# Performance work log

Hardware: AMD Instinct MI355X
Metric: run time of the kernel (lower is better)

The kernel has to match this reference:

```python
import jax, jax.numpy as jnp
import numpy as np

B, T, H = 4096, 2048, 64  # batch, max seq len, hidden size
IN = 1                    # decoder input hardcoded to width 1 in source
BOT = 3                   # latent bottleneck (linear_enc: H->3, linear_dec: 3->H)


def setup_inputs() -> dict:
    key = jax.random.key(0)
    ks = jax.random.split(key, 16)
    s = 1.0 / np.sqrt(H)
    u = lambda k, shape: jax.random.uniform(k, shape, jnp.float32, -s, s)
    padded = jax.random.normal(ks[0], (B, T, IN), jnp.float32)
    seq_lengths = jax.random.randint(ks[1], (B,), 1, T + 1).at[0].set(T)  # max == T (static unroll)
    return {
        "padded": padded,
        "seq_lengths": seq_lengths,
        # encoder LSTM (gate order i,f,g,o like torch); biases b_ih+b_hh fused
        "enc_Wih": u(ks[2], (4 * H, IN)),
        "enc_Whh": u(ks[3], (4 * H, H)),
        "enc_b":   u(ks[4], (4 * H,)),
        # encoder bottleneck linear H->3
        "enc_linW": u(ks[5], (BOT, H)),
        "enc_linb": u(ks[6], (BOT,)),
        # decoder expand linear 3->H
        "dec_linW": u(ks[7], (H, BOT)),
        "dec_linb": u(ks[8], (H,)),
        # decoder LSTM
        "dec_Wih": u(ks[9], (4 * H, IN)),
        "dec_Whh": u(ks[10], (4 * H, H)),
        "dec_b":   u(ks[11], (4 * H,)),
        # output linear H->1
        "outW": u(ks[12], (IN, H)),
        "outb": u(ks[13], (IN,)),
    }


def _lstm_cell(x, h, c, Wih, Whh, b):
    g = x @ Wih.T + h @ Whh.T + b
    i, f, gg, o = jnp.split(g, 4, axis=-1)
    c = jax.nn.sigmoid(f) * c + jax.nn.sigmoid(i) * jnp.tanh(gg)
    h = jax.nn.sigmoid(o) * jnp.tanh(c)
    return h, c


def reference(padded, seq_lengths, enc_Wih, enc_Whh, enc_b, enc_linW, enc_linb,
              dec_linW, dec_linb, dec_Wih, dec_Whh, dec_b, outW, outb):
    Bn, Tn, _ = padded.shape
    Hn = enc_Whh.shape[1]
    xs = jnp.transpose(padded, (1, 0, 2))                       # (T, B, 1)
    mask = jnp.arange(Tn)[:, None] < seq_lengths[None, :]        # (T, B)

    # ---- encoder: packed semantics == freeze (h,c) past each seq's length ----
    h0 = jnp.zeros((Bn, Hn), padded.dtype)
    def enc_step(carry, xm):
        h, c = carry
        x, m = xm
        nh, nc = _lstm_cell(x, h, c, enc_Wih, enc_Whh, enc_b)
        m = m[:, None]
        return (jnp.where(m, nh, h), jnp.where(m, nc, c)), None
    (h, c), _ = jax.lax.scan(enc_step, (h0, h0), (xs, mask))

    hz = jax.nn.sigmoid(h @ enc_linW.T + enc_linb)               # (B, 3) latent

    hd = hz @ dec_linW.T + dec_linb                              # (B, H)
    x0 = jnp.zeros((Bn, 1), padded.dtype)
    def dec_step(carry, _):
        x, hh, cc = carry
        nh, nc = _lstm_cell(x, hh, cc, dec_Wih, dec_Whh, dec_b)
        y = nh @ outW.T + outb
        return (y, nh, nc), y
    _, ys = jax.lax.scan(dec_step, (x0, hd, c), None, length=Tn)  # (T, B, 1)
    output = jnp.transpose(ys, (1, 0, 2))                         # (B, T, 1)

    # ---- masked MSE ----
    maskf = mask.T[:, :, None].astype(padded.dtype)               # (B, T, 1)
    loss = (((padded - output) ** 2) * maskf).sum() / maskf.sum()
    return loss, padded, output, hz[None]
```

## Files before the change

### kernel.cpp

```cpp
#include <hip/hip_runtime.h>

#define B 4096
#define T 2048
#define H 64
#define NBATCH 16
#define NB (B / NBATCH)
#define NTHREADS 512

typedef __attribute__((ext_vector_type(8))) short short8;
typedef __attribute__((ext_vector_type(4))) float f32x4;

__device__ __forceinline__ float ex2(float x) { return __builtin_amdgcn_exp2f(x); }
__device__ __forceinline__ float sigm(float x) {
    return __builtin_amdgcn_rcpf(1.0f + ex2(-1.4426950408889634f * x));
}
__device__ __forceinline__ float tanh_(float x) {
    return __builtin_fmaf(2.0f,
        __builtin_amdgcn_rcpf(1.0f + ex2(-2.8853900817779268f * x)), -1.0f);
}
__device__ __forceinline__ unsigned short f2bf(float f) {
    unsigned u = __builtin_bit_cast(unsigned, f);
    u += 0x7fffu + ((u >> 16) & 1u);
    return (unsigned short)(u >> 16);
}
__device__ __forceinline__ unsigned pk_bf16(float a, float b) {
    unsigned r;
    asm("v_cvt_pk_bf16_f32 %0, %1, %2" : "=v"(r) : "v"(a), "v"(b));
    return r;
}
__device__ __forceinline__ void lds_barrier() {
    asm volatile("s_waitcnt lgkmcnt(0)\n\ts_barrier" ::: "memory");
}

extern "C" __global__ void __launch_bounds__(NTHREADS, 2)
enc_kernel(const float* __restrict__ padded, const int* __restrict__ seq_len,
           const float* __restrict__ Wih, const float* __restrict__ Whh,
           const float* __restrict__ bias,
           float* __restrict__ h_out, float* __restrict__ c_out)
{
    __shared__ unsigned short hX[2][NBATCH][72];
    __shared__ int slen[NBATCH];

    const int tid = threadIdx.x;
    const int w = tid >> 6, L = tid & 63, lo = L & 15, hi = L >> 4;
    const int b0 = blockIdx.x * NBATCH;
    const int unitA = w * 8 + hi;
    const int unitB = w * 8 + 4 + hi;

    short8 af[2][2];
    #pragma unroll
    for (int rt = 0; rt < 2; ++rt) {
        const int G = (lo & 3) * 64 + w * 8 + rt * 4 + (lo >> 2);
        #pragma unroll
        for (int kk = 0; kk < 2; ++kk) {
            const float* src = Whh + (long)G * H + kk * 32 + hi * 8;
            short8 f;
            #pragma unroll
            for (int j = 0; j < 8; ++j) f[j] = (short)f2bf(src[j]);
            af[rt][kk] = f;
        }
    }
    float b_g[2][4], wi_g[2][4];
    #pragma unroll
    for (int rt = 0; rt < 2; ++rt)
        #pragma unroll
        for (int r = 0; r < 4; ++r) {
            const int G2 = r * 64 + w * 8 + rt * 4 + hi;
            b_g[rt][r] = bias[G2];
            wi_g[rt][r] = Wih[G2];
        }

    #pragma unroll
    for (int idx = tid; idx < NBATCH * 64; idx += NTHREADS)
        hX[0][idx >> 6][idx & 63] = 0;
    if (tid < NBATCH) slen[tid] = seq_len[b0 + tid];
    lds_barrier();

    int maxlen = 1;
    #pragma unroll
    for (int i = 0; i < NBATCH; ++i) maxlen = max(maxlen, slen[i]);
    const int len_lo = slen[lo];

    const float* xrow = padded + (long)(b0 + lo) * T;
    f32x4 xc = *(const f32x4*)(xrow);
    f32x4 xn = *(const f32x4*)(xrow + 4);

    float csA = 0.f, hsA = 0.f, csB = 0.f, hsB = 0.f;

#define ESTEP(P, XI)                                                          \
    {                                                                         \
        const float x = xc[XI];                                               \
        short8 hb0 = *(const short8*)&hX[P][lo][hi * 8];                      \
        short8 hb1 = *(const short8*)&hX[P][lo][32 + hi * 8];                 \
        f32x4 z0 = {b_g[0][0] + wi_g[0][0] * x, b_g[0][1] + wi_g[0][1] * x,   \
                    b_g[0][2] + wi_g[0][2] * x, b_g[0][3] + wi_g[0][3] * x};  \
        f32x4 z1 = {b_g[1][0] + wi_g[1][0] * x, b_g[1][1] + wi_g[1][1] * x,   \
                    b_g[1][2] + wi_g[1][2] * x, b_g[1][3] + wi_g[1][3] * x};  \
        z0 = __builtin_amdgcn_mfma_f32_16x16x32_bf16(af[0][0], hb0, z0, 0,0,0); \
        z1 = __builtin_amdgcn_mfma_f32_16x16x32_bf16(af[1][0], hb0, z1, 0,0,0); \
        z0 = __builtin_amdgcn_mfma_f32_16x16x32_bf16(af[0][1], hb1, z0, 0,0,0); \
        z1 = __builtin_amdgcn_mfma_f32_16x16x32_bf16(af[1][1], hb1, z1, 0,0,0); \
        const bool act = (t + XI) < len_lo;                                   \
        float iA = sigm(z0[0]), fA = sigm(z0[1]);                             \
        float gA = tanh_(z0[2]), oA = sigm(z0[3]);                            \
        float iB = sigm(z1[0]), fB = sigm(z1[1]);                             \
        float gB = tanh_(z1[2]), oB = sigm(z1[3]);                            \
        float cnA = fA * csA + iA * gA;                                       \
        float cnB = fB * csB + iB * gB;                                       \
        float hnA = oA * tanh_(cnA);                                          \
        float hnB = oB * tanh_(cnB);                                          \
        if (act) { csA = cnA; hsA = hnA; csB = cnB; hsB = hnB; }              \
        unsigned up = pk_bf16(hsA, hsB);                                      \
        hX[(P) ^ 1][lo][unitA] = (unsigned short)up;                          \
        hX[(P) ^ 1][lo][unitB] = (unsigned short)(up >> 16);                  \
        lds_barrier();                                                        \
    }

    for (int t = 0; t < maxlen; t += 4) {
        int nb = t + 8; if (nb > T - 4) nb = T - 4;
        f32x4 xf = *(const f32x4*)(xrow + nb);
        ESTEP(0, 0) ESTEP(1, 1) ESTEP(0, 2) ESTEP(1, 3)
        xc = xn; xn = xf;
    }
#undef ESTEP

    h_out[(long)(b0 + lo) * H + unitA] = hsA;
    h_out[(long)(b0 + lo) * H + unitB] = hsB;
    c_out[(long)(b0 + lo) * H + unitA] = csA;
    c_out[(long)(b0 + lo) * H + unitB] = csB;
}

extern "C" __global__ void __launch_bounds__(256)
mid_kernel(const float* __restrict__ h_enc,
           const float* __restrict__ eW, const float* __restrict__ eb,
           const float* __restrict__ dW, const float* __restrict__ db,
           const float* __restrict__ outW, const float* __restrict__ outb,
           float* __restrict__ hz_out, float* __restrict__ hd_out,
           float* __restrict__ y0c)
{
    int b = blockIdx.x * blockDim.x + threadIdx.x;
    if (b >= B) return;
    const float* h = h_enc + (long)b * H;
    float hz[3];
    #pragma unroll
    for (int j = 0; j < 3; ++j) {
        float s = eb[j];
        for (int k = 0; k < H; ++k) s += h[k] * eW[j*H + k];
        hz[j] = sigm(s);
        hz_out[b*3 + j] = hz[j];
    }
    float y0 = outb[0];
    for (int u = 0; u < H; ++u) {
        float hd = db[u] + hz[0]*dW[u*3] + hz[1]*dW[u*3+1] + hz[2]*dW[u*3+2];
        hd_out[(long)b*H + u] = hd;
        y0 += outW[u] * hd;
    }
    y0c[b] = y0;
}

extern "C" __global__ void __launch_bounds__(NTHREADS, 2)
dec_kernel(const float* __restrict__ hd, const float* __restrict__ c_in,
           const float* __restrict__ Wih, const float* __restrict__ Whh,
           const float* __restrict__ bias, const float* __restrict__ outW,
           const float* __restrict__ outb, const float* __restrict__ y0c,
           float* __restrict__ y_out)
{
    __shared__ unsigned short hX[2][NBATCH][72];

    const int tid = threadIdx.x;
    const int w = tid >> 6, L = tid & 63, lo = L & 15, hi = L >> 4;
    const int b0 = blockIdx.x * NBATCH;
    const int unitA = w * 8 + hi;
    const int unitB = w * 8 + 4 + hi;

    short8 af[2][2];
    #pragma unroll
    for (int rt = 0; rt < 2; ++rt) {
        const int G = (lo & 3) * 64 + w * 8 + rt * 4 + (lo >> 2);
        const float wir = Wih[G];
        #pragma unroll
        for (int kk = 0; kk < 2; ++kk) {
            const float* src = Whh + (long)G * H + kk * 32 + hi * 8;
            const float* ow  = outW + kk * 32 + hi * 8;
            short8 f;
            #pragma unroll
            for (int j = 0; j < 8; ++j) f[j] = (short)f2bf(src[j] + wir * ow[j]);
            af[rt][kk] = f;
        }
    }
    const float outb_s = outb[0];
    const float y0 = y0c[b0 + lo];
    float zb[2][4], corr[2][4];
    #pragma unroll
    for (int rt = 0; rt < 2; ++rt)
        #pragma unroll
        for (int r = 0; r < 4; ++r) {
            const int G2 = r * 64 + w * 8 + rt * 4 + hi;
            zb[rt][r] = bias[G2] + Wih[G2] * outb_s;
            corr[rt][r] = Wih[G2] * y0;
        }

    short8 ya[2];
    #pragma unroll
    for (int kk = 0; kk < 2; ++kk) {
        short8 f = (short8)0;
        if (lo == 0)
            #pragma unroll
            for (int j = 0; j < 8; ++j) f[j] = (short)f2bf(outW[kk*32 + hi*8 + j]);
        ya[kk] = f;
    }

    #pragma unroll
    for (int idx = tid; idx < NBATCH * 64; idx += NTHREADS)
        hX[0][idx >> 6][idx & 63] = f2bf(hd[(long)(b0 + (idx >> 6)) * H + (idx & 63)]);
    float csA = c_in[(long)(b0 + lo) * H + unitA];
    float csB = c_in[(long)(b0 + lo) * H + unitB];
    lds_barrier();

#define DSTEP(P, CORR, TT)                                                    \
    {                                                                         \
        short8 hb0 = *(const short8*)&hX[P][lo][hi * 8];                      \
        short8 hb1 = *(const short8*)&hX[P][lo][32 + hi * 8];                 \
        f32x4 z0 = {zb[0][0], zb[0][1], zb[0][2], zb[0][3]};                  \
        f32x4 z1 = {zb[1][0], zb[1][1], zb[1][2], zb[1][3]};                  \
        z0 = __builtin_amdgcn_mfma_f32_16x16x32_bf16(af[0][0], hb0, z0, 0,0,0); \
        z1 = __builtin_amdgcn_mfma_f32_16x16x32_bf16(af[1][0], hb0, z1, 0,0,0); \
        z0 = __builtin_amdgcn_mfma_f32_16x16x32_bf16(af[0][1], hb1, z0, 0,0,0); \
        z1 = __builtin_amdgcn_mfma_f32_16x16x32_bf16(af[1][1], hb1, z1, 0,0,0); \
        if (w == ((TT) & 7)) {      \
            f32x4 zy = {outb_s, outb_s, outb_s, outb_s};                      \
            zy = __builtin_amdgcn_mfma_f32_16x16x32_bf16(ya[0], hb0, zy, 0,0,0); \
            zy = __builtin_amdgcn_mfma_f32_16x16x32_bf16(ya[1], hb1, zy, 0,0,0); \
            if ((TT) > 0 && hi == 0)                                          \
                y_out[(long)(b0 + lo) * T + ((TT) - 1)] = zy[0];              \
        }                                                                     \
        if (CORR) {                                                           \
            _Pragma("unroll")                                                 \
            for (int r = 0; r < 4; ++r) { z0[r] -= corr[0][r]; z1[r] -= corr[1][r]; } \
        }                                                                     \
        float iA = sigm(z0[0]), fA = sigm(z0[1]);                             \
        float gA = tanh_(z0[2]), oA = sigm(z0[3]);                            \
        float iB = sigm(z1[0]), fB = sigm(z1[1]);                             \
        float gB = tanh_(z1[2]), oB = sigm(z1[3]);                            \
        float cnA = fA * csA + iA * gA;                                       \
        float cnB = fB * csB + iB * gB;                                       \
        float hnA = oA * tanh_(cnA);                                          \
        float hnB = oB * tanh_(cnB);                                          \
        csA = cnA; csB = cnB;                                                 \
        unsigned up = pk_bf16(hnA, hnB);                                      \
        hX[(P) ^ 1][lo][unitA] = (unsigned short)up;                          \
        hX[(P) ^ 1][lo][unitB] = (unsigned short)(up >> 16);                  \
        lds_barrier();                                                        \
    }

    DSTEP(0, 1, 0) DSTEP(1, 0, 1) DSTEP(0, 0, 2) DSTEP(1, 0, 3)
    for (int t = 4; t < T; t += 4) {
        DSTEP(0, 0, t) DSTEP(1, 0, t + 1) DSTEP(0, 0, t + 2) DSTEP(1, 0, t + 3)
    }
#undef DSTEP

    if (w == 0) {
        short8 hb0 = *(const short8*)&hX[0][lo][hi * 8];
        short8 hb1 = *(const short8*)&hX[0][lo][32 + hi * 8];
        f32x4 zy = {outb_s, outb_s, outb_s, outb_s};
        zy = __builtin_amdgcn_mfma_f32_16x16x32_bf16(ya[0], hb0, zy, 0,0,0);
        zy = __builtin_amdgcn_mfma_f32_16x16x32_bf16(ya[1], hb1, zy, 0,0,0);
        if (hi == 0) y_out[(long)(b0 + lo) * T + (T - 1)] = zy[0];
    }
}

extern "C" __global__ void __launch_bounds__(256)
loss_kernel(const float* __restrict__ padded, const float* __restrict__ y,
            const int* __restrict__ seq_len, float* __restrict__ acc2)
{
    const long n4 = (long)B * T / 4;
    long i0 = (long)(blockIdx.x * blockDim.x + threadIdx.x);
    long stride = (long)gridDim.x * blockDim.x;
    float s = 0.f, cnt = 0.f;
    for (long i = i0; i < n4; i += stride) {
        int b = (int)(i >> 9);
        int t = (int)(i & 511) * 4;
        int len = seq_len[b];
        f32x4 pv = *(const f32x4*)&padded[i * 4];
        f32x4 yv = *(const f32x4*)&y[i * 4];
        #pragma unroll
        for (int e = 0; e < 4; ++e)
            if (t + e < len) { float d = pv[e] - yv[e]; s += d * d; cnt += 1.0f; }
    }
    for (int m = 1; m < 64; m <<= 1) { s += __shfl_xor(s, m); cnt += __shfl_xor(cnt, m); }
    if ((threadIdx.x & 63) == 0) { atomicAdd(&acc2[0], s); atomicAdd(&acc2[1], cnt); }
}

extern "C" __global__ void fin_kernel(const float* __restrict__ acc2, float* __restrict__ out)
{
    out[0] = acc2[0] / acc2[1];
}

extern "C" void kernel_launch(void* const* d_in, const int* in_sizes, int n_in,
                              void* d_out, int out_size, void* d_ws, size_t ws_size,
                              hipStream_t stream)
{
    const float* padded = (const float*)d_in[0];
    const int*   seq    = (const int*)  d_in[1];
    const float* eWih   = (const float*)d_in[2];
    const float* eWhh   = (const float*)d_in[3];
    const float* eb     = (const float*)d_in[4];
    const float* elW    = (const float*)d_in[5];
    const float* elb    = (const float*)d_in[6];
    const float* dlW    = (const float*)d_in[7];
    const float* dlb    = (const float*)d_in[8];
    const float* dWih   = (const float*)d_in[9];
    const float* dWhh   = (const float*)d_in[10];
    const float* db     = (const float*)d_in[11];
    const float* outW   = (const float*)d_in[12];
    const float* outb   = (const float*)d_in[13];
    float* out = (float*)d_out;

    float* ws    = (float*)d_ws;
    float* h_enc = ws;
    float* c_enc = ws + (long)B * H;
    float* hd    = ws + 2L * B * H;
    float* y0c   = ws + 3L * B * H;
    float* acc2  = ws + 3L * B * H + B;

    float* out_pad = out + 1;
    float* out_y   = out + 1 + (long)B * T;
    float* out_hz  = out + 1 + 2L * (long)B * T;

    hipMemcpyAsync(out_pad, padded, (long)B * T * sizeof(float),
                   hipMemcpyDeviceToDevice, stream);
    hipMemsetAsync(acc2, 0, 2 * sizeof(float), stream);

    enc_kernel<<<NB, NTHREADS, 0, stream>>>(padded, seq, eWih, eWhh, eb, h_enc, c_enc);
    mid_kernel<<<B / 256, 256, 0, stream>>>(h_enc, elW, elb, dlW, dlb, outW, outb,
                                            out_hz, hd, y0c);
    dec_kernel<<<NB, NTHREADS, 0, stream>>>(hd, c_enc, dWih, dWhh, db, outW, outb, y0c, out_y);
    loss_kernel<<<1024, 256, 0, stream>>>(padded, out_y, seq, acc2);
    fin_kernel<<<1, 1, 0, stream>>>(acc2, out);
}
```

Before: 1.828 ms.

## Split batch into two interleaved halves to overlap MFMA with gate activations

Each block's 16 sequences are split into two groups of 8 that alternate phases. While one group's gate matmul runs on MFMA, the other group's sigmoid/tanh and cell update run, so the recurrent dependency chain of one half hides behind the other. The lane layout changes so each lane handles one hidden unit for one batch row in each half, which halves the activation work per phase. The cost is more barriers per timestep pair, a more complex y-output indexing schedule and more register state, with a risk of off-by-one errors in the masking and output timing.

```diff
diff --git a/kernel.cpp b/kernel.cpp
--- a/kernel.cpp
+++ b/kernel.cpp
@@ -23,11 +23,6 @@
     u += 0x7fffu + ((u >> 16) & 1u);
     return (unsigned short)(u >> 16);
 }
-__device__ __forceinline__ unsigned pk_bf16(float a, float b) {
-    unsigned r;
-    asm("v_cvt_pk_bf16_f32 %0, %1, %2" : "=v"(r) : "v"(a), "v"(b));
-    return r;
-}
 __device__ __forceinline__ void lds_barrier() {
     asm volatile("s_waitcnt lgkmcnt(0)\n\ts_barrier" ::: "memory");
 }
@@ -38,19 +33,20 @@
            const float* __restrict__ bias,
            float* __restrict__ h_out, float* __restrict__ c_out)
 {
-    __shared__ unsigned short hX[2][NBATCH][72];
+    __shared__ unsigned short hX[2][8][80];
     __shared__ int slen[NBATCH];
 
     const int tid = threadIdx.x;
-    const int w = tid >> 6, L = tid & 63, lo = L & 15, hi = L >> 4;
+    const int w = tid >> 6, L = tid & 63, c = L & 15, hi = L >> 4;
     const int b0 = blockIdx.x * NBATCH;
-    const int unitA = w * 8 + hi;
-    const int unitB = w * 8 + 4 + hi;
+    const int cb = c & 7;
+    const int rsel = c >> 3;
+    const int u = w * 8 + rsel * 4 + hi;
 
     short8 af[2][2];
     #pragma unroll
     for (int rt = 0; rt < 2; ++rt) {
-        const int G = (lo & 3) * 64 + w * 8 + rt * 4 + (lo >> 2);
+        const int G = (c & 3) * 64 + w * 8 + rt * 4 + (c >> 2);
         #pragma unroll
         for (int kk = 0; kk < 2; ++kk) {
             const float* src = Whh + (long)G * H + kk * 32 + hi * 8;
@@ -70,28 +66,43 @@
             wi_g[rt][r] = Wih[G2];
         }
 
-    #pragma unroll
-    for (int idx = tid; idx < NBATCH * 64; idx += NTHREADS)
-        hX[0][idx >> 6][idx & 63] = 0;
+    for (int idx = tid; idx < 2 * 8 * 80; idx += NTHREADS)
+        ((unsigned short*)hX)[idx] = 0;
     if (tid < NBATCH) slen[tid] = seq_len[b0 + tid];
     lds_barrier();
 
     int maxlen = 1;
     #pragma unroll
     for (int i = 0; i < NBATCH; ++i) maxlen = max(maxlen, slen[i]);
-    const int len_lo = slen[lo];
-
-    const float* xrow = padded + (long)(b0 + lo) * T;
-    f32x4 xc = *(const f32x4*)(xrow);
-    f32x4 xn = *(const f32x4*)(xrow + 4);
-
-    float csA = 0.f, hsA = 0.f, csB = 0.f, hsB = 0.f;
-
-#define ESTEP(P, XI)                                                          \
+    const int len0 = slen[cb];
+    const int len1 = slen[8 + cb];
+
+    const float* xrow0 = padded + (long)(b0 + cb) * T;
+    const float* xrow1 = padded + (long)(b0 + 8 + cb) * T;
+    f32x4 xc0 = *(const f32x4*)(xrow0), xn0 = *(const f32x4*)(xrow0 + 4);
+    f32x4 xc1 = *(const f32x4*)(xrow1), xn1 = *(const f32x4*)(xrow1 + 4);
+
+    float cs0 = 0.f, hs0 = 0.f, cs1 = 0.f, hs1 = 0.f;
+    f32x4 gz00 = {0.f,0.f,0.f,0.f}, gz01 = {0.f,0.f,0.f,0.f};
+    f32x4 gz10 = {0.f,0.f,0.f,0.f}, gz11 = {0.f,0.f,0.f,0.f};
+
+#define REV(I)                                                                \
     {                                                                         \
-        const float x = xc[XI];                                               \
-        short8 hb0 = *(const short8*)&hX[P][lo][hi * 8];                      \
-        short8 hb1 = *(const short8*)&hX[P][lo][32 + hi * 8];                 \
+        short8 hb0 = *(const short8*)&hX[0][cb][hi * 8];                      \
+        short8 hb1 = *(const short8*)&hX[0][cb][32 + hi * 8];                 \
+        {                                                                     \
+            float a0 = rsel ? gz11[0] : gz10[0];                              \
+            float a1 = rsel ? gz11[1] : gz10[1];                              \
+            float a2 = rsel ? gz11[2] : gz10[2];                              \
+            float a3 = rsel ? gz11[3] : gz10[3];                              \
+            float i_ = sigm(a0), f_ = sigm(a1);                               \
+            float g_ = tanh_(a2), o_ = sigm(a3);                              \
+            float cn = f_ * cs1 + i_ * g_;                                    \
+            float hn = o_ * tanh_(cn);                                        \
+            if ((t + (I) - 1) < len1) { cs1 = cn; hs1 = hn; }                 \
+            hX[1][cb][u] = f2bf(hs1);                                         \
+        }                                                                     \
+        const float x = xc0[I];                                               \
         f32x4 z0 = {b_g[0][0] + wi_g[0][0] * x, b_g[0][1] + wi_g[0][1] * x,   \
                     b_g[0][2] + wi_g[0][2] * x, b_g[0][3] + wi_g[0][3] * x};  \
         f32x4 z1 = {b_g[1][0] + wi_g[1][0] * x, b_g[1][1] + wi_g[1][1] * x,   \
@@ -100,34 +111,66 @@
         z1 = __builtin_amdgcn_mfma_f32_16x16x32_bf16(af[1][0], hb0, z1, 0,0,0); \
         z0 = __builtin_amdgcn_mfma_f32_16x16x32_bf16(af[0][1], hb1, z0, 0,0,0); \
         z1 = __builtin_amdgcn_mfma_f32_16x16x32_bf16(af[1][1], hb1, z1, 0,0,0); \
-        const bool act = (t + XI) < len_lo;                                   \
-        float iA = sigm(z0[0]), fA = sigm(z0[1]);                             \
-        float gA = tanh_(z0[2]), oA = sigm(z0[3]);                            \
-        float iB = sigm(z1[0]), fB = sigm(z1[1]);                             \
-        float gB = tanh_(z1[2]), oB = sigm(z1[3]);                            \
-        float cnA = fA * csA + iA * gA;                                       \
-        float cnB = fB * csB + iB * gB;                                       \
-        float hnA = oA * tanh_(cnA);                                          \
-        float hnB = oB * tanh_(cnB);                                          \
-        if (act) { csA = cnA; hsA = hnA; csB = cnB; hsB = hnB; }              \
-        unsigned up = pk_bf16(hsA, hsB);                                      \
-        hX[(P) ^ 1][lo][unitA] = (unsigned short)up;                          \
-        hX[(P) ^ 1][lo][unitB] = (unsigned short)(up >> 16);                  \
+        gz00 = z0; gz01 = z1;                                                 \
         lds_barrier();                                                        \
     }
 
-    for (int t = 0; t < maxlen; t += 4) {
+#define ROD(I)                                                                \
+    {                                                                         \
+        short8 hb0 = *(const short8*)&hX[1][cb][hi * 8];                      \
+        short8 hb1 = *(const short8*)&hX[1][cb][32 + hi * 8];                 \
+        {                                                                     \
+            float a0 = rsel ? gz01[0] : gz00[0];                              \
+            float a1 = rsel ? gz01[1] : gz00[1];                              \
+            float a2 = rsel ? gz01[2] : gz00[2];                              \
+            float a3 = rsel ? gz01[3] : gz00[3];                              \
+            float i_ = sigm(a0), f_ = sigm(a1);                               \
+            float g_ = tanh_(a2), o_ = sigm(a3);                              \
+            float cn = f_ * cs0 + i_ * g_;                                    \
+            float hn = o_ * tanh_(cn);                                        \
+            if ((t + (I)) < len0) { cs0 = cn; hs0 = hn; }                     \
+            hX[0][cb][u] = f2bf(hs0);                                         \
+        }                                                                     \
+        const float x = xc1[I];                                               \
+        f32x4 z0 = {b_g[0][0] + wi_g[0][0] * x, b_g[0][1] + wi_g[0][1] * x,   \
+                    b_g[0][2] + wi_g[0][2] * x, b_g[0][3] + wi_g[0][3] * x};  \
+        f32x4 z1 = {b_g[1][0] + wi_g[1][0] * x, b_g[1][1] + wi_g[1][1] * x,   \
+                    b_g[1][2] + wi_g[1][2] * x, b_g[1][3] + wi_g[1][3] * x};  \
+        z0 = __builtin_amdgcn_mfma_f32_16x16x32_bf16(af[0][0], hb0, z0, 0,0,0); \
+        z1 = __builtin_amdgcn_mfma_f32_16x16x32_bf16(af[1][0], hb0, z1, 0,0,0); \
+        z0 = __builtin_amdgcn_mfma_f32_16x16x32_bf16(af[0][1], hb1, z0, 0,0,0); \
+        z1 = __builtin_amdgcn_mfma_f32_16x16x32_bf16(af[1][1], hb1, z1, 0,0,0); \
+        gz10 = z0; gz11 = z1;                                                 \
+        lds_barrier();                                                        \
+    }
+
+    int t = 0;
+    for (; t < maxlen; t += 4) {
         int nb = t + 8; if (nb > T - 4) nb = T - 4;
-        f32x4 xf = *(const f32x4*)(xrow + nb);
-        ESTEP(0, 0) ESTEP(1, 1) ESTEP(0, 2) ESTEP(1, 3)
-        xc = xn; xn = xf;
-    }
-#undef ESTEP
-
-    h_out[(long)(b0 + lo) * H + unitA] = hsA;
-    h_out[(long)(b0 + lo) * H + unitB] = hsB;
-    c_out[(long)(b0 + lo) * H + unitA] = csA;
-    c_out[(long)(b0 + lo) * H + unitB] = csB;
+        f32x4 xf0 = *(const f32x4*)(xrow0 + nb);
+        f32x4 xf1 = *(const f32x4*)(xrow1 + nb);
+        REV(0) ROD(0) REV(1) ROD(1) REV(2) ROD(2) REV(3) ROD(3)
+        xc0 = xn0; xn0 = xf0;
+        xc1 = xn1; xn1 = xf1;
+    }
+#undef REV
+#undef ROD
+    {
+        float a0 = rsel ? gz11[0] : gz10[0];
+        float a1 = rsel ? gz11[1] : gz10[1];
+        float a2 = rsel ? gz11[2] : gz10[2];
+        float a3 = rsel ? gz11[3] : gz10[3];
+        float i_ = sigm(a0), f_ = sigm(a1);
+        float g_ = tanh_(a2), o_ = sigm(a3);
+        float cn = f_ * cs1 + i_ * g_;
+        float hn = o_ * tanh_(cn);
+        if ((t - 1) < len1) { cs1 = cn; hs1 = hn; }
+    }
+
+    h_out[(long)(b0 + cb) * H + u] = hs0;
+    c_out[(long)(b0 + cb) * H + u] = cs0;
+    h_out[(long)(b0 + 8 + cb) * H + u] = hs1;
+    c_out[(long)(b0 + 8 + cb) * H + u] = cs1;
 }
 
 extern "C" __global__ void __launch_bounds__(256)
@@ -165,18 +208,19 @@
            const float* __restrict__ outb, const float* __restrict__ y0c,
            float* __restrict__ y_out)
 {
-    __shared__ unsigned short hX[2][NBATCH][72];
+    __shared__ unsigned short hX[2][8][80];
 
     const int tid = threadIdx.x;
-    const int w = tid >> 6, L = tid & 63, lo = L & 15, hi = L >> 4;
+    const int w = tid >> 6, L = tid & 63, c = L & 15, hi = L >> 4;
     const int b0 = blockIdx.x * NBATCH;
-    const int unitA = w * 8 + hi;
-    const int unitB = w * 8 + 4 + hi;
+    const int cb = c & 7;
+    const int rsel = c >> 3;
+    const int u = w * 8 + rsel * 4 + hi;
 
     short8 af[2][2];
     #pragma unroll
     for (int rt = 0; rt < 2; ++rt) {
-        const int G = (lo & 3) * 64 + w * 8 + rt * 4 + (lo >> 2);
+        const int G = (c & 3) * 64 + w * 8 + rt * 4 + (c >> 2);
         const float wir = Wih[G];
         #pragma unroll
         for (int kk = 0; kk < 2; ++kk) {
@@ -189,83 +233,135 @@
         }
     }
     const float outb_s = outb[0];
-    const float y0 = y0c[b0 + lo];
-    float zb[2][4], corr[2][4];
+    const float y00 = y0c[b0 + cb];
+    const float y01 = y0c[b0 + 8 + cb];
+    float zb[2][4], wih_a[4];
     #pragma unroll
     for (int rt = 0; rt < 2; ++rt)
         #pragma unroll
         for (int r = 0; r < 4; ++r) {
             const int G2 = r * 64 + w * 8 + rt * 4 + hi;
             zb[rt][r] = bias[G2] + Wih[G2] * outb_s;
-            corr[rt][r] = Wih[G2] * y0;
         }
+    #pragma unroll
+    for (int r = 0; r < 4; ++r) wih_a[r] = Wih[r * 64 + u];
 
     short8 ya[2];
     #pragma unroll
     for (int kk = 0; kk < 2; ++kk) {
         short8 f = (short8)0;
-        if (lo == 0)
+        if (c == 0)
             #pragma unroll
             for (int j = 0; j < 8; ++j) f[j] = (short)f2bf(outW[kk*32 + hi*8 + j]);
         ya[kk] = f;
     }
 
-    #pragma unroll
-    for (int idx = tid; idx < NBATCH * 64; idx += NTHREADS)
-        hX[0][idx >> 6][idx & 63] = f2bf(hd[(long)(b0 + (idx >> 6)) * H + (idx & 63)]);
-    float csA = c_in[(long)(b0 + lo) * H + unitA];
-    float csB = c_in[(long)(b0 + lo) * H + unitB];
+    for (int idx = tid; idx < 1024; idx += NTHREADS) {
+        int p = idx >> 9, m = (idx >> 6) & 7, k = idx & 63;
+        hX[p][m][k] = f2bf(hd[(long)(b0 + 8 * p + m) * H + k]);
+    }
+    float cs0 = c_in[(long)(b0 + cb) * H + u];
+    float cs1 = c_in[(long)(b0 + 8 + cb) * H + u];
+    f32x4 gz00, gz01, gz10, gz11;
     lds_barrier();
 
-#define DSTEP(P, CORR, TT)                                                    \
+    {
+        short8 hb0 = *(const short8*)&hX[0][cb][hi * 8];
+        short8 hb1 = *(const short8*)&hX[0][cb][32 + hi * 8];
+        f32x4 z0 = {zb[0][0], zb[0][1], zb[0][2], zb[0][3]};
+        f32x4 z1 = {zb[1][0], zb[1][1], zb[1][2], zb[1][3]};
+        z0 = __builtin_amdgcn_mfma_f32_16x16x32_bf16(af[0][0], hb0, z0, 0,0,0);
+        z1 = __builtin_amdgcn_mfma_f32_16x16x32_bf16(af[1][0], hb0, z1, 0,0,0);
+        z0 = __builtin_amdgcn_mfma_f32_16x16x32_bf16(af[0][1], hb1, z0, 0,0,0);
+        z1 = __builtin_amdgcn_mfma_f32_16x16x32_bf16(af[1][1], hb1, z1, 0,0,0);
+        gz00 = z0; gz01 = z1;
+        lds_barrier();
+    }
+
+#define DRE(TT, CF)                                                           \
     {                                                                         \
-        short8 hb0 = *(const short8*)&hX[P][lo][hi * 8];                      \
-        short8 hb1 = *(const short8*)&hX[P][lo][32 + hi * 8];                 \
+        short8 hb0 = *(const short8*)&hX[1][cb][hi * 8];                      \
+        short8 hb1 = *(const short8*)&hX[1][cb][32 + hi * 8];                 \
+        {                                                                     \
+            float a0 = rsel ? gz01[0] : gz00[0];                              \
+            float a1 = rsel ? gz01[1] : gz00[1];                              \
+            float a2 = rsel ? gz01[2] : gz00[2];                              \
+            float a3 = rsel ? gz01[3] : gz00[3];                              \
+            if (CF) { a0 -= wih_a[0] * y00; a1 -= wih_a[1] * y00;             \
+                      a2 -= wih_a[2] * y00; a3 -= wih_a[3] * y00; }           \
+            float i_ = sigm(a0), f_ = sigm(a1);                               \
+            float g_ = tanh_(a2), o_ = sigm(a3);                              \
+            float cn = f_ * cs0 + i_ * g_;                                    \
+            float hn = o_ * tanh_(cn);                                        \
+            cs0 = cn;                                                         \
+            hX[0][cb][u] = f2bf(hn);                                          \
+        }                                                                     \
         f32x4 z0 = {zb[0][0], zb[0][1], zb[0][2], zb[0][3]};                  \
         f32x4 z1 = {zb[1][0], zb[1][1], zb[1][2], zb[1][3]};                  \
         z0 = __builtin_amdgcn_mfma_f32_16x16x32_bf16(af[0][0], hb0, z0, 0,0,0); \
         z1 = __builtin_amdgcn_mfma_f32_16x16x32_bf16(af[1][0], hb0, z1, 0,0,0); \
         z0 = __builtin_amdgcn_mfma_f32_16x16x32_bf16(af[0][1], hb1, z0, 0,0,0); \
         z1 = __builtin_amdgcn_mfma_f32_16x16x32_bf16(af[1][1], hb1, z1, 0,0,0); \
-        if (w == ((TT) & 7)) {      \
+        gz10 = z0; gz11 = z1;                                                 \
+        if (!(CF) && w == ((TT) & 7)) {                                       \
             f32x4 zy = {outb_s, outb_s, outb_s, outb_s};                      \
             zy = __builtin_amdgcn_mfma_f32_16x16x32_bf16(ya[0], hb0, zy, 0,0,0); \
             zy = __builtin_amdgcn_mfma_f32_16x16x32_bf16(ya[1], hb1, zy, 0,0,0); \
-            if ((TT) > 0 && hi == 0)                                          \
-                y_out[(long)(b0 + lo) * T + ((TT) - 1)] = zy[0];              \
-        }                                                                     \
-        if (CORR) {                                                           \
-            _Pragma("unroll")                                                 \
-            for (int r = 0; r < 4; ++r) { z0[r] -= corr[0][r]; z1[r] -= corr[1][r]; } \
-        }                                                                     \
-        float iA = sigm(z0[0]), fA = sigm(z0[1]);                             \
-        float gA = tanh_(z0[2]), oA = sigm(z0[3]);                            \
-        float iB = sigm(z1[0]), fB = sigm(z1[1]);                             \
-        float gB = tanh_(z1[2]), oB = sigm(z1[3]);                            \
-        float cnA = fA * csA + iA * gA;                                       \
-        float cnB = fB * csB + iB * gB;                                       \
-        float hnA = oA * tanh_(cnA);                                          \
-        float hnB = oB * tanh_(cnB);                                          \
-        csA = cnA; csB = cnB;                                                 \
-        unsigned up = pk_bf16(hnA, hnB);                                      \
-        hX[(P) ^ 1][lo][unitA] = (unsigned short)up;                          \
-        hX[(P) ^ 1][lo][unitB] = (unsigned short)(up >> 16);                  \
+            if (hi == 0 && c < 8)                                             \
+                y_out[(long)(b0 + 8 + cb) * T + ((TT) - 1)] = zy[0];          \
+        }                                                                     \
         lds_barrier();                                                        \
     }
 
-    DSTEP(0, 1, 0) DSTEP(1, 0, 1) DSTEP(0, 0, 2) DSTEP(1, 0, 3)
-    for (int t = 4; t < T; t += 4) {
-        DSTEP(0, 0, t) DSTEP(1, 0, t + 1) DSTEP(0, 0, t + 2) DSTEP(1, 0, t + 3)
-    }
-#undef DSTEP
+#define DRO(TT, CF)                                                           \
+    {                                                                         \
+        short8 hb0 = *(const short8*)&hX[0][cb][hi * 8];                      \
+        short8 hb1 = *(const short8*)&hX[0][cb][32 + hi * 8];                 \
+        {                                                                     \
+            float a0 = rsel ? gz11[0] : gz10[0];                              \
+            float a1 = rsel ? gz11[1] : gz10[1];                              \
+            float a2 = rsel ? gz11[2] : gz10[2];                              \
+            float a3 = rsel ? gz11[3] : gz10[3];                              \
+            if (CF) { a0 -= wih_a[0] * y01; a1 -= wih_a[1] * y01;             \
+                      a2 -= wih_a[2] * y01; a3 -= wih_a[3] * y01; }           \
+            float i_ = sigm(a0), f_ = sigm(a1);                               \
+            float g_ = tanh_(a2), o_ = sigm(a3);                              \
+            float cn = f_ * cs1 + i_ * g_;                                    \
+            float hn = o_ * tanh_(cn);                                        \
+            cs1 = cn;                                                         \
+            hX[1][cb][u] = f2bf(hn);                                          \
+        }                                                                     \
+        f32x4 z0 = {zb[0][0], zb[0][1], zb[0][2], zb[0][3]};                  \
+        f32x4 z1 = {zb[1][0], zb[1][1], zb[1][2], zb[1][3]};                  \
+        z0 = __builtin_amdgcn_mfma_f32_16x16x32_bf16(af[0][0], hb0, z0, 0,0,0); \
+        z1 = __builtin_amdgcn_mfma_f32_16x16x32_bf16(af[1][0], hb0, z1, 0,0,0); \
+        z0 = __builtin_amdgcn_mfma_f32_16x16x32_bf16(af[0][1], hb1, z0, 0,0,0); \
+        z1 = __builtin_amdgcn_mfma_f32_16x16x32_bf16(af[1][1], hb1, z1, 0,0,0); \
+        gz00 = z0; gz01 = z1;                                                 \
+        if (w == (((TT) + 1) & 7)) {                                          \
+            f32x4 zy = {outb_s, outb_s, outb_s, outb_s};                      \
+            zy = __builtin_amdgcn_mfma_f32_16x16x32_bf16(ya[0], hb0, zy, 0,0,0); \
+            zy = __builtin_amdgcn_mfma_f32_16x16x32_bf16(ya[1], hb1, zy, 0,0,0); \
+            if (hi == 0 && c < 8)                                             \
+                y_out[(long)(b0 + cb) * T + (TT)] = zy[0];                    \
+        }                                                                     \
+        lds_barrier();                                                        \
+    }
+
+    DRE(0, 1) DRO(0, 1) DRE(1, 0) DRO(1, 0)
+    for (int m = 2; m < T; m += 2) {
+        DRE(m, 0) DRO(m, 0) DRE(m + 1, 0) DRO(m + 1, 0)
+    }
+#undef DRE
+#undef DRO
 
     if (w == 0) {
-        short8 hb0 = *(const short8*)&hX[0][lo][hi * 8];
-        short8 hb1 = *(const short8*)&hX[0][lo][32 + hi * 8];
+        short8 hb0 = *(const short8*)&hX[1][cb][hi * 8];
+        short8 hb1 = *(const short8*)&hX[1][cb][32 + hi * 8];
         f32x4 zy = {outb_s, outb_s, outb_s, outb_s};
         zy = __builtin_amdgcn_mfma_f32_16x16x32_bf16(ya[0], hb0, zy, 0,0,0);
         zy = __builtin_amdgcn_mfma_f32_16x16x32_bf16(ya[1], hb1, zy, 0,0,0);
-        if (hi == 0) y_out[(long)(b0 + lo) * T + (T - 1)] = zy[0];
+        if (hi == 0 && c < 8) y_out[(long)(b0 + 8 + cb) * T + (T - 1)] = zy[0];
     }
 }
 
```

Result: slower. 2.412 ms (+32.0%).

## Merge LSTM gate reciprocals and pack adjacent hidden units for single LDS stores

Applied to the files above, without the earlier changes.

Rewrites the LSTM cell so that i*tanh(g) and o*tanh(c) each use one combined reciprocal over the product of denominators, which cuts the count of rcp operations per cell. The cell state is clamped before the tanh exponent to avoid overflow. Gate rows are remapped so each lane owns two adjacent hidden units, turning two 16-bit LDS stores into one 32-bit store and making the final h/c global writes float2. The aim is to shorten the serial per-step critical path, at the cost of slightly different rounding and a clamp that changes results only for extreme cell states.

```diff
diff --git a/kernel.cpp b/kernel.cpp
--- a/kernel.cpp
+++ b/kernel.cpp
@@ -11,13 +11,6 @@
 typedef __attribute__((ext_vector_type(4))) float f32x4;
 
 __device__ __forceinline__ float ex2(float x) { return __builtin_amdgcn_exp2f(x); }
-__device__ __forceinline__ float sigm(float x) {
-    return __builtin_amdgcn_rcpf(1.0f + ex2(-1.4426950408889634f * x));
-}
-__device__ __forceinline__ float tanh_(float x) {
-    return __builtin_fmaf(2.0f,
-        __builtin_amdgcn_rcpf(1.0f + ex2(-2.8853900817779268f * x)), -1.0f);
-}
 __device__ __forceinline__ unsigned short f2bf(float f) {
     unsigned u = __builtin_bit_cast(unsigned, f);
     u += 0x7fffu + ((u >> 16) & 1u);
@@ -30,6 +23,22 @@
 }
 __device__ __forceinline__ void lds_barrier() {
     asm volatile("s_waitcnt lgkmcnt(0)\n\ts_barrier" ::: "memory");
+}
+
+__device__ __forceinline__ void cellstep(const f32x4 z, float& cs, float& hs, bool act) {
+    const float KE = -1.4426950408889634f;
+    const float KT = -2.8853900817779268f;
+    float pf = ex2(KE * z[1]);
+    float f_ = __builtin_amdgcn_rcpf(1.0f + pf);
+    float p0 = ex2(KE * z[0]);
+    float v_ = ex2(KT * z[2]);
+    float ig = (1.0f - v_) * __builtin_amdgcn_rcpf((1.0f + p0) * (1.0f + v_));
+    float cn = __builtin_fmaf(f_, cs, ig);
+    float cc = fminf(15.0f, fmaxf(-15.0f, cn));
+    float s_ = ex2(KE * z[3]);
+    float r_ = ex2(KT * cc);
+    float hn = (1.0f - r_) * __builtin_amdgcn_rcpf((1.0f + s_) * (1.0f + r_));
+    if (act) { cs = cn; hs = hn; }
 }
 
 extern "C" __global__ void __launch_bounds__(NTHREADS, 2)
@@ -44,13 +53,13 @@
     const int tid = threadIdx.x;
     const int w = tid >> 6, L = tid & 63, lo = L & 15, hi = L >> 4;
     const int b0 = blockIdx.x * NBATCH;
-    const int unitA = w * 8 + hi;
-    const int unitB = w * 8 + 4 + hi;
+    const int unitA = w * 8 + 2 * hi;
+    const int unitB = unitA + 1;
 
     short8 af[2][2];
     #pragma unroll
     for (int rt = 0; rt < 2; ++rt) {
-        const int G = (lo & 3) * 64 + w * 8 + rt * 4 + (lo >> 2);
+        const int G = (lo & 3) * 64 + w * 8 + 2 * (lo >> 2) + rt;
         #pragma unroll
         for (int kk = 0; kk < 2; ++kk) {
             const float* src = Whh + (long)G * H + kk * 32 + hi * 8;
@@ -65,12 +74,11 @@
     for (int rt = 0; rt < 2; ++rt)
         #pragma unroll
         for (int r = 0; r < 4; ++r) {
-            const int G2 = r * 64 + w * 8 + rt * 4 + hi;
+            const int G2 = r * 64 + w * 8 + 2 * hi + rt;
             b_g[rt][r] = bias[G2];
             wi_g[rt][r] = Wih[G2];
         }
 
-    #pragma unroll
     for (int idx = tid; idx < NBATCH * 64; idx += NTHREADS)
         hX[0][idx >> 6][idx & 63] = 0;
     if (tid < NBATCH) slen[tid] = seq_len[b0 + tid];
@@ -101,18 +109,9 @@
         z0 = __builtin_amdgcn_mfma_f32_16x16x32_bf16(af[0][1], hb1, z0, 0,0,0); \
         z1 = __builtin_amdgcn_mfma_f32_16x16x32_bf16(af[1][1], hb1, z1, 0,0,0); \
         const bool act = (t + XI) < len_lo;                                   \
-        float iA = sigm(z0[0]), fA = sigm(z0[1]);                             \
-        float gA = tanh_(z0[2]), oA = sigm(z0[3]);                            \
-        float iB = sigm(z1[0]), fB = sigm(z1[1]);                             \
-        float gB = tanh_(z1[2]), oB = sigm(z1[3]);                            \
-        float cnA = fA * csA + iA * gA;                                       \
-        float cnB = fB * csB + iB * gB;                                       \
-        float hnA = oA * tanh_(cnA);                                          \
-        float hnB = oB * tanh_(cnB);                                          \
-        if (act) { csA = cnA; hsA = hnA; csB = cnB; hsB = hnB; }              \
-        unsigned up = pk_bf16(hsA, hsB);                                      \
-        hX[(P) ^ 1][lo][unitA] = (unsigned short)up;                          \
-        hX[(P) ^ 1][lo][unitB] = (unsigned short)(up >> 16);                  \
+        cellstep(z0, csA, hsA, act);                                          \
+        cellstep(z1, csB, hsB, act);                                          \
+        *(unsigned*)&hX[(P) ^ 1][lo][unitA] = pk_bf16(hsA, hsB);              \
         lds_barrier();                                                        \
     }
 
@@ -124,10 +123,8 @@
     }
 #undef ESTEP
 
-    h_out[(long)(b0 + lo) * H + unitA] = hsA;
-    h_out[(long)(b0 + lo) * H + unitB] = hsB;
-    c_out[(long)(b0 + lo) * H + unitA] = csA;
-    c_out[(long)(b0 + lo) * H + unitB] = csB;
+    *(float2*)&h_out[(long)(b0 + lo) * H + unitA] = make_float2(hsA, hsB);
+    *(float2*)&c_out[(long)(b0 + lo) * H + unitA] = make_float2(csA, csB);
 }
 
 extern "C" __global__ void __launch_bounds__(256)
@@ -146,7 +143,7 @@
     for (int j = 0; j < 3; ++j) {
         float s = eb[j];
         for (int k = 0; k < H; ++k) s += h[k] * eW[j*H + k];
-        hz[j] = sigm(s);
+        hz[j] = 1.0f / (1.0f + __builtin_expf(-s));
         hz_out[b*3 + j] = hz[j];
     }
     float y0 = outb[0];
@@ -170,13 +167,13 @@
     const int tid = threadIdx.x;
     const int w = tid >> 6, L = tid & 63, lo = L & 15, hi = L >> 4;
     const int b0 = blockIdx.x * NBATCH;
-    const int unitA = w * 8 + hi;
-    const int unitB = w * 8 + 4 + hi;
+    const int unitA = w * 8 + 2 * hi;
+    const int unitB = unitA + 1;
 
     short8 af[2][2];
     #pragma unroll
     for (int rt = 0; rt < 2; ++rt) {
-        const int G = (lo & 3) * 64 + w * 8 + rt * 4 + (lo >> 2);
+        const int G = (lo & 3) * 64 + w * 8 + 2 * (lo >> 2) + rt;
         const float wir = Wih[G];
         #pragma unroll
         for (int kk = 0; kk < 2; ++kk) {
@@ -195,7 +192,7 @@
     for (int rt = 0; rt < 2; ++rt)
         #pragma unroll
         for (int r = 0; r < 4; ++r) {
-            const int G2 = r * 64 + w * 8 + rt * 4 + hi;
+            const int G2 = r * 64 + w * 8 + 2 * hi + rt;
             zb[rt][r] = bias[G2] + Wih[G2] * outb_s;
             corr[rt][r] = Wih[G2] * y0;
         }
@@ -210,11 +207,10 @@
         ya[kk] = f;
     }
 
-    #pragma unroll
     for (int idx = tid; idx < NBATCH * 64; idx += NTHREADS)
         hX[0][idx >> 6][idx & 63] = f2bf(hd[(long)(b0 + (idx >> 6)) * H + (idx & 63)]);
-    float csA = c_in[(long)(b0 + lo) * H + unitA];
-    float csB = c_in[(long)(b0 + lo) * H + unitB];
+    float2 c2 = *(const float2*)&c_in[(long)(b0 + lo) * H + unitA];
+    float csA = c2.x, csB = c2.y, hsA = 0.f, hsB = 0.f;
     lds_barrier();
 
 #define DSTEP(P, CORR, TT)                                                    \
@@ -238,18 +234,9 @@
             _Pragma("unroll")                                                 \
             for (int r = 0; r < 4; ++r) { z0[r] -= corr[0][r]; z1[r] -= corr[1][r]; } \
         }                                                                     \
-        float iA = sigm(z0[0]), fA = sigm(z0[1]);                             \
-        float gA = tanh_(z0[2]), oA = sigm(z0[3]);                            \
-        float iB = sigm(z1[0]), fB = sigm(z1[1]);                             \
-        float gB = tanh_(z1[2]), oB = sigm(z1[3]);                            \
-        float cnA = fA * csA + iA * gA;                                       \
-        float cnB = fB * csB + iB * gB;                                       \
-        float hnA = oA * tanh_(cnA);                                          \
-        float hnB = oB * tanh_(cnB);                                          \
-        csA = cnA; csB = cnB;                                                 \
-        unsigned up = pk_bf16(hnA, hnB);                                      \
-        hX[(P) ^ 1][lo][unitA] = (unsigned short)up;                          \
-        hX[(P) ^ 1][lo][unitB] = (unsigned short)(up >> 16);                  \
+        cellstep(z0, csA, hsA, true);                                         \
+        cellstep(z1, csB, hsB, true);                                         \
+        *(unsigned*)&hX[(P) ^ 1][lo][unitA] = pk_bf16(hsA, hsB);              \
         lds_barrier();                                                        \
     }
 
```

Result: no change. 1.806 ms (-1.2%).
